# Kernel tuning notes

Hardware: AMD Instinct MI355X
Metric: run time of the kernel (lower is better)

Reference implementation:

```python
import jax, jax.numpy as jnp
import numpy as np

D_MODEL = 1024
HEADS = 16


def setup_inputs() -> dict:
    key = jax.random.key(0)
    ks = jax.random.split(key, 5)
    S = 4096
    x = jax.random.normal(ks[0], (S, D_MODEL), dtype=jnp.float32)
    scale = 1.0 / np.sqrt(D_MODEL)
    Wq = jax.random.normal(ks[1], (D_MODEL, D_MODEL), dtype=jnp.float32) * scale
    Wk = jax.random.normal(ks[2], (D_MODEL, D_MODEL), dtype=jnp.float32) * scale
    Wv = jax.random.normal(ks[3], (D_MODEL, D_MODEL), dtype=jnp.float32) * scale
    Wo = jax.random.normal(ks[4], (D_MODEL, D_MODEL), dtype=jnp.float32) * scale
    return {"x": x, "Wq": Wq, "Wk": Wk, "Wv": Wv, "Wo": Wo}


def reference(x, Wq, Wk, Wv, Wo):
    # x: [S, D]; weights follow torch Linear convention y = x @ W.T
    S, D = x.shape
    H = HEADS
    d_k = D // H
    q = (x @ Wq.T).reshape(S, H, d_k)  # [S,H,dk]
    k = (x @ Wk.T).reshape(S, H, d_k)
    v = (x @ Wv.T).reshape(S, H, d_k)
    # logits: [H, S, S] = q k^T / sqrt(d_k)
    logits = jnp.einsum('shd,thd->hst', q, k) / jnp.sqrt(jnp.asarray(d_k, x.dtype))
    probs = jax.nn.softmax(logits, axis=-1)
    out = jnp.einsum('hst,thd->shd', probs, v).reshape(S, D)
    return out @ Wo.T
```

## Files before the change

### kernel.cpp

```cpp
#include <hip/hip_runtime.h>
#include <hip/hip_bf16.h>


typedef __bf16 bf16_t;
typedef __bf16 bf16x8 __attribute__((ext_vector_type(8)));
typedef __bf16 bf16x4 __attribute__((ext_vector_type(4)));
typedef float f32x4 __attribute__((ext_vector_type(4)));

#define D_MODEL 1024
#define SEQ 4096
#define HEADS 16
#define DK 64
#define QSCALE 0.1803368801111204f
#define EXP2_MAGIC 8404859.0f

__global__ void cast_all(const float* __restrict__ x, const float* __restrict__ a,
                         const float* __restrict__ b, const float* __restrict__ c,
                         const float* __restrict__ d, bf16_t* __restrict__ xb,
                         bf16_t* __restrict__ wb) {
    const int gi = blockIdx.x * blockDim.x + threadIdx.x;
    const float* src; bf16_t* dst; int i;
    if (gi < SEQ * D_MODEL / 4) {
        src = x; dst = xb; i = gi * 4;
    } else {
        int g = gi - SEQ * D_MODEL / 4;
        int which = g >> 18;
        src = which == 0 ? a : which == 1 ? b : which == 2 ? c : d;
        dst = wb + (size_t)which * D_MODEL * D_MODEL;
        i = (g & 0x3FFFF) * 4;
    }
    float4 v = *(const float4*)(src + i);
    bf16x4 o;
    o[0] = (bf16_t)v.x; o[1] = (bf16_t)v.y; o[2] = (bf16_t)v.z; o[3] = (bf16_t)v.w;
    *(bf16x4*)(dst + i) = o;
}

__device__ __forceinline__ void g2l16(const bf16_t* g, bf16_t* l) {
    __builtin_amdgcn_global_load_lds(
        (const __attribute__((address_space(1))) void*)g,
        (__attribute__((address_space(3))) void*)l, 16, 0, 0);
}

__device__ __forceinline__ bf16x8 exp2_pk(const f32x4 a, const f32x4 b) {
    union { float f; unsigned u; } v[8];
#pragma unroll
    for (int r = 0; r < 4; r++) {
        v[r].f     = fmaf(a[r], 128.0f, EXP2_MAGIC);
        v[r + 4].f = fmaf(b[r], 128.0f, EXP2_MAGIC);
    }
    union { unsigned u[4]; bf16x8 h; } o;
#pragma unroll
    for (int p = 0; p < 4; p++)
        o.u[p] = __builtin_amdgcn_perm(v[2 * p + 1].u, v[2 * p].u, 0x05040100u);
    return o.h;
}

template <int ROUTE>
__global__ __launch_bounds__(256, 2) void gemm_lds(const bf16_t* __restrict__ A,
                                                   const bf16_t* __restrict__ B,
                                                   void* __restrict__ out0,
                                                   void* __restrict__ out1,
                                                   void* __restrict__ out2,
                                                   int M, int N, int K) {
    __shared__ __align__(16) bf16_t As[128 * 64];
    __shared__ __align__(16) bf16_t Bs[128 * 64];

    const int tid = threadIdx.x;
    const int lane = tid & 63;
    const int wave = tid >> 6;
    const int l15 = lane & 15;
    const int lg  = lane >> 4;

    const int flat = blockIdx.y * gridDim.x + blockIdx.x;
    const int mpx  = gridDim.y >> 3;
    const int xcd  = flat & 7;
    const int pos  = flat >> 3;
    const int m0 = (xcd * mpx + (pos % mpx)) * 128;
    const int n0 = (pos / mpx) * 128;
    const int wm = (wave >> 1) * 64;
    const int wn = (wave & 1) * 64;

    const bf16_t* aSrc[4]; bf16_t* aDst[4];
    const bf16_t* bSrc[4]; bf16_t* bDst[4];
#pragma unroll
    for (int it = 0; it < 4; it++) {
        int c = it * 256 + tid;
        int row = c >> 3, cc = (c & 7) ^ (row & 7);
        aSrc[it] = A + (size_t)(m0 + row) * K + cc * 8;
        aDst[it] = As + c * 8;
        bSrc[it] = B + (size_t)(n0 + row) * K + cc * 8;
        bDst[it] = Bs + c * 8;
    }

    int aoff[2][4], boff[2][4];
#pragma unroll
    for (int kk = 0; kk < 2; kk++) {
#pragma unroll
        for (int i = 0; i < 4; i++) {
            int row = wm + i * 16 + l15;
            aoff[kk][i] = row * 64 + (((kk << 2) | lg) ^ (row & 7)) * 8;
        }
#pragma unroll
        for (int j = 0; j < 4; j++) {
            int row = wn + j * 16 + l15;
            boff[kk][j] = row * 64 + (((kk << 2) | lg) ^ (row & 7)) * 8;
        }
    }

    f32x4 acc[4][4];
#pragma unroll
    for (int i = 0; i < 4; i++)
#pragma unroll
        for (int j = 0; j < 4; j++) acc[i][j] = f32x4{0.f, 0.f, 0.f, 0.f};

    for (int k0 = 0; k0 < K; k0 += 64) {
#pragma unroll
        for (int it = 0; it < 4; it++) g2l16(aSrc[it] + k0, aDst[it]);
#pragma unroll
        for (int it = 0; it < 4; it++) g2l16(bSrc[it] + k0, bDst[it]);
        __syncthreads();

#pragma unroll
        for (int kk = 0; kk < 2; kk++) {
            bf16x8 af[4], bfm[4];
#pragma unroll
            for (int i = 0; i < 4; i++) af[i] = *(const bf16x8*)(As + aoff[kk][i]);
#pragma unroll
            for (int j = 0; j < 4; j++) bfm[j] = *(const bf16x8*)(Bs + boff[kk][j]);
#pragma unroll
            for (int i = 0; i < 4; i++)
#pragma unroll
                for (int j = 0; j < 4; j++)
                    acc[i][j] = __builtin_amdgcn_mfma_f32_16x16x32_bf16(af[i], bfm[j], acc[i][j], 0, 0, 0);
        }
        __syncthreads();
    }

    const int ng = n0 + wn;
    if (ROUTE == 0) {
        float* C = (float*)out0;
#pragma unroll
        for (int i = 0; i < 4; i++)
#pragma unroll
            for (int r = 0; r < 4; r++) {
                int m = m0 + wm + i * 16 + lg * 4 + r;
                float* crow = C + (size_t)m * N + ng;
#pragma unroll
                for (int j = 0; j < 4; j++) crow[j * 16 + l15] = acc[i][j][r];
            }
    } else {
        if (ng < 2048) {
            const bool isQ = (ng < 1024);
            const float sc = isQ ? QSCALE : 1.0f;
            bf16_t* dst = isQ ? (bf16_t*)out0 : (bf16_t*)out1;
            int nn = ng & 1023;
#pragma unroll
            for (int i = 0; i < 4; i++)
#pragma unroll
                for (int r = 0; r < 4; r++) {
                    int m = m0 + wm + i * 16 + lg * 4 + r;
                    bf16_t* crow = dst + (size_t)m * D_MODEL + nn;
#pragma unroll
                    for (int j = 0; j < 4; j++) crow[j * 16 + l15] = (bf16_t)(acc[i][j][r] * sc);
                }
        } else {
            bf16_t* Vt = (bf16_t*)out2;
#pragma unroll
            for (int i = 0; i < 4; i++)
#pragma unroll
                for (int j = 0; j < 4; j++) {
                    int vcol = ng - 2048 + j * 16 + l15;
                    int m = m0 + wm + i * 16 + lg * 4;
                    int mp = (m & ~31) | (((m >> 2) & 3) << 3) | (((m >> 4) & 1) << 2);
                    bf16x4 v4;
#pragma unroll
                    for (int r = 0; r < 4; r++) v4[r] = (bf16_t)acc[i][j][r];
                    *(bf16x4*)(Vt + (size_t)vcol * SEQ + mp) = v4;
                }
        }
    }
}

__global__ __launch_bounds__(512, 2) void attn_kernel(const bf16_t* __restrict__ Q,
                                                      const bf16_t* __restrict__ Km,
                                                      const bf16_t* __restrict__ Vt,
                                                      bf16_t* __restrict__ O) {
    const int tid = threadIdx.x;
    const int lane = tid & 63;
    const int wave = tid >> 6;
    const int l15 = lane & 15;
    const int lg  = lane >> 4;
    const int bid = blockIdx.x;
    const int h    = (bid & 7) * 2 + ((bid >> 3) & 1);
    const int qblk = bid >> 4;
    const int q0 = qblk * 256;
    const int hoff = h * DK;

    __shared__ struct {
        __align__(16) bf16_t K[2][64 * 64];
        __align__(16) bf16_t V[2][64 * 64];
    } sm;

    bf16x8 qf[2][2];
#pragma unroll
    for (int t = 0; t < 2; t++)
#pragma unroll
        for (int c = 0; c < 2; c++)
            qf[t][c] = *(const bf16x8*)(Q + (size_t)(q0 + wave * 32 + t * 16 + l15) * D_MODEL
                                        + hoff + c * 32 + lg * 8);

    f32x4 oacc[2][4], lfrag[2];
#pragma unroll
    for (int t = 0; t < 2; t++) {
        lfrag[t] = f32x4{0.f, 0.f, 0.f, 0.f};
#pragma unroll
        for (int dt = 0; dt < 4; dt++) oacc[t][dt] = f32x4{0.f, 0.f, 0.f, 0.f};
    }

    bf16x8 ones8;
#pragma unroll
    for (int j = 0; j < 8; j++) ones8[j] = (bf16_t)1.0f;

    const int srow = tid >> 3;
    const int sdc = (tid & 7) ^ (srow & 7);
    const bf16_t* kSrc = Km + (size_t)srow * D_MODEL + hoff + sdc * 8;
    const bf16_t* vSrc = Vt + (size_t)(hoff + srow) * SEQ + sdc * 8;

    int kOff[4][2], vOff[2][4];
#pragma unroll
    for (int kt = 0; kt < 4; kt++)
#pragma unroll
        for (int c = 0; c < 2; c++) {
            int row = kt * 16 + l15;
            kOff[kt][c] = row * 64 + (((c * 4 + lg) ^ (row & 7)) * 8);
        }
#pragma unroll
    for (int kp = 0; kp < 2; kp++)
#pragma unroll
        for (int dt = 0; dt < 4; dt++) {
            int row = dt * 16 + l15;
            vOff[kp][dt] = row * 64 + (((kp * 4 + lg) ^ (row & 7)) * 8);
        }

    g2l16(kSrc, &sm.K[0][tid * 8]);
    g2l16(vSrc, &sm.V[0][tid * 8]);

    for (int s = 0; s < SEQ / 64; s++) {
        const int cur = s & 1;
        __syncthreads();

        if (s + 1 < SEQ / 64) {
            const int nxt = cur ^ 1;
            g2l16(kSrc + (size_t)(s + 1) * 64 * D_MODEL, &sm.K[nxt][tid * 8]);
            g2l16(vSrc + (s + 1) * 64,                   &sm.V[nxt][tid * 8]);
        }

        const bf16_t* Kb = sm.K[cur];
        const bf16_t* Vb = sm.V[cur];

#pragma unroll
        for (int kp = 0; kp < 2; kp++) {
            bf16x8 vf[4];
#pragma unroll
            for (int dt = 0; dt < 4; dt++) vf[dt] = *(const bf16x8*)(Vb + vOff[kp][dt]);

            f32x4 st[2][2];
#pragma unroll
            for (int sub = 0; sub < 2; sub++) {
                const int kt = kp * 2 + sub;
                const bf16x8 kf0 = *(const bf16x8*)(Kb + kOff[kt][0]);
                const bf16x8 kf1 = *(const bf16x8*)(Kb + kOff[kt][1]);
#pragma unroll
                for (int t = 0; t < 2; t++) {
                    f32x4 a = f32x4{0.f, 0.f, 0.f, 0.f};
                    a = __builtin_amdgcn_mfma_f32_16x16x32_bf16(kf0, qf[t][0], a, 0, 0, 0);
                    a = __builtin_amdgcn_mfma_f32_16x16x32_bf16(kf1, qf[t][1], a, 0, 0, 0);
                    st[t][sub] = a;
                }
            }

#pragma unroll
            for (int t = 0; t < 2; t++) {
                const bf16x8 pbig = exp2_pk(st[t][0], st[t][1]);
                lfrag[t] = __builtin_amdgcn_mfma_f32_16x16x32_bf16(ones8, pbig, lfrag[t], 0, 0, 0);
#pragma unroll
                for (int dt = 0; dt < 4; dt++)
                    oacc[t][dt] = __builtin_amdgcn_mfma_f32_16x16x32_bf16(vf[dt], pbig, oacc[t][dt], 0, 0, 0);
            }
        }
    }

#pragma unroll
    for (int t = 0; t < 2; t++) {
        const float inv = 1.f / lfrag[t][0];
        const size_t qrow = (size_t)(q0 + wave * 32 + t * 16 + l15);
#pragma unroll
        for (int dt = 0; dt < 4; dt++) {
            bf16x4 o4;
#pragma unroll
            for (int r = 0; r < 4; r++) o4[r] = (bf16_t)(oacc[t][dt][r] * inv);
            *(bf16x4*)(O + qrow * D_MODEL + hoff + dt * 16 + lg * 4) = o4;
        }
    }
}

extern "C" void kernel_launch(void* const* d_in, const int* in_sizes, int n_in,
                              void* d_out, int out_size, void* d_ws, size_t ws_size,
                              hipStream_t stream) {
    const float* x  = (const float*)d_in[0];
    const float* Wq = (const float*)d_in[1];
    const float* Wk = (const float*)d_in[2];
    const float* Wv = (const float*)d_in[3];
    const float* Wo = (const float*)d_in[4];
    float* out = (float*)d_out;

    char* ws = (char*)d_ws;
    bf16_t* xb  = (bf16_t*)(ws);
    bf16_t* wqb = (bf16_t*)(ws + (8u  << 20));
    bf16_t* wob = (bf16_t*)(ws + (14u << 20));
    bf16_t* Qb  = (bf16_t*)(ws + (16u << 20));
    bf16_t* Kb  = (bf16_t*)(ws + (24u << 20));
    bf16_t* Vtb = (bf16_t*)(ws + (32u << 20));
    bf16_t* Ab  = (bf16_t*)(ws + (40u << 20));

    cast_all<<<8192, 256, 0, stream>>>(x, Wq, Wk, Wv, Wo, xb, wqb);

    gemm_lds<1><<<dim3(3 * D_MODEL / 128, SEQ / 128), 256, 0, stream>>>(
        xb, wqb, Qb, Kb, Vtb, SEQ, 3 * D_MODEL, D_MODEL);

    attn_kernel<<<256, 512, 0, stream>>>(Qb, Kb, Vtb, Ab);

    gemm_lds<0><<<dim3(D_MODEL / 128, SEQ / 128), 256, 0, stream>>>(
        Ab, wob, out, nullptr, nullptr, SEQ, D_MODEL, D_MODEL);
}
```

Baseline: 185.4 us.

## Fuse fp32-to-bf16 casts into GEMM tile loads and drop cast kernel

Removes the separate cast_all kernel and has the QKV and output-projection GEMMs read fp32 inputs and weights directly, converting to bf16 in registers before writing swizzled LDS tiles. This saves one launch and the write-then-reread of bf16 copies of x and the weights. The cost is twice the global read bytes per tile, repeated conversion work across the blocks that share a tile, and synchronous register-staged loads in place of the async global_load_lds path, which may stall the MFMA loop.

```diff
diff --git a/kernel.cpp b/kernel.cpp
--- a/kernel.cpp
+++ b/kernel.cpp
@@ -14,27 +14,6 @@
 #define QSCALE 0.1803368801111204f
 #define EXP2_MAGIC 8404859.0f
 
-__global__ void cast_all(const float* __restrict__ x, const float* __restrict__ a,
-                         const float* __restrict__ b, const float* __restrict__ c,
-                         const float* __restrict__ d, bf16_t* __restrict__ xb,
-                         bf16_t* __restrict__ wb) {
-    const int gi = blockIdx.x * blockDim.x + threadIdx.x;
-    const float* src; bf16_t* dst; int i;
-    if (gi < SEQ * D_MODEL / 4) {
-        src = x; dst = xb; i = gi * 4;
-    } else {
-        int g = gi - SEQ * D_MODEL / 4;
-        int which = g >> 18;
-        src = which == 0 ? a : which == 1 ? b : which == 2 ? c : d;
-        dst = wb + (size_t)which * D_MODEL * D_MODEL;
-        i = (g & 0x3FFFF) * 4;
-    }
-    float4 v = *(const float4*)(src + i);
-    bf16x4 o;
-    o[0] = (bf16_t)v.x; o[1] = (bf16_t)v.y; o[2] = (bf16_t)v.z; o[3] = (bf16_t)v.w;
-    *(bf16x4*)(dst + i) = o;
-}
-
 __device__ __forceinline__ void g2l16(const bf16_t* g, bf16_t* l) {
     __builtin_amdgcn_global_load_lds(
         (const __attribute__((address_space(1))) void*)g,
@@ -55,13 +34,21 @@
     return o.h;
 }
 
-template <int ROUTE>
-__global__ __launch_bounds__(256, 2) void gemm_lds(const bf16_t* __restrict__ A,
-                                                   const bf16_t* __restrict__ B,
-                                                   void* __restrict__ out0,
-                                                   void* __restrict__ out1,
-                                                   void* __restrict__ out2,
-                                                   int M, int N, int K) {
+__device__ __forceinline__ bf16x8 cvt8(const float4 p0, const float4 p1) {
+    bf16x8 w;
+    w[0] = (bf16_t)p0.x; w[1] = (bf16_t)p0.y; w[2] = (bf16_t)p0.z; w[3] = (bf16_t)p0.w;
+    w[4] = (bf16_t)p1.x; w[5] = (bf16_t)p1.y; w[6] = (bf16_t)p1.z; w[7] = (bf16_t)p1.w;
+    return w;
+}
+
+__global__ __launch_bounds__(256) void gemm_qkv(const float* __restrict__ X,
+                                                const float* __restrict__ Wq,
+                                                const float* __restrict__ Wk,
+                                                const float* __restrict__ Wv,
+                                                bf16_t* __restrict__ Qb,
+                                                bf16_t* __restrict__ Kb,
+                                                bf16_t* __restrict__ Vt) {
+    const int K = D_MODEL;
     __shared__ __align__(16) bf16_t As[128 * 64];
     __shared__ __align__(16) bf16_t Bs[128 * 64];
 
@@ -80,16 +67,19 @@
     const int wm = (wave >> 1) * 64;
     const int wn = (wave & 1) * 64;
 
-    const bf16_t* aSrc[4]; bf16_t* aDst[4];
-    const bf16_t* bSrc[4]; bf16_t* bDst[4];
+    const float* Wsel = (n0 < 1024) ? Wq : (n0 < 2048) ? Wk : Wv;
+    const int nb = n0 & 1023;
+
+    const float* aS[4]; const float* bS[4];
+    bf16_t* aD[4]; bf16_t* bD[4];
 #pragma unroll
     for (int it = 0; it < 4; it++) {
         int c = it * 256 + tid;
-        int row = c >> 3, cc = (c & 7) ^ (row & 7);
-        aSrc[it] = A + (size_t)(m0 + row) * K + cc * 8;
-        aDst[it] = As + c * 8;
-        bSrc[it] = B + (size_t)(n0 + row) * K + cc * 8;
-        bDst[it] = Bs + c * 8;
+        int row = c >> 3, j0 = c & 7, cc = j0 ^ (row & 7);
+        aS[it] = X    + (size_t)(m0 + row) * K + j0 * 8;
+        bS[it] = Wsel + (size_t)(nb + row) * K + j0 * 8;
+        aD[it] = As + row * 64 + cc * 8;
+        bD[it] = Bs + row * 64 + cc * 8;
     }
 
     int aoff[2][4], boff[2][4];
@@ -115,9 +105,17 @@
 
     for (int k0 = 0; k0 < K; k0 += 64) {
 #pragma unroll
-        for (int it = 0; it < 4; it++) g2l16(aSrc[it] + k0, aDst[it]);
-#pragma unroll
-        for (int it = 0; it < 4; it++) g2l16(bSrc[it] + k0, bDst[it]);
+        for (int it = 0; it < 4; it++) {
+            float4 p0 = *(const float4*)(aS[it] + k0);
+            float4 p1 = *(const float4*)(aS[it] + k0 + 4);
+            *(bf16x8*)aD[it] = cvt8(p0, p1);
+        }
+#pragma unroll
+        for (int it = 0; it < 4; it++) {
+            float4 p0 = *(const float4*)(bS[it] + k0);
+            float4 p1 = *(const float4*)(bS[it] + k0 + 4);
+            *(bf16x8*)bD[it] = cvt8(p0, p1);
+        }
         __syncthreads();
 
 #pragma unroll
@@ -137,48 +135,128 @@
     }
 
     const int ng = n0 + wn;
-    if (ROUTE == 0) {
-        float* C = (float*)out0;
+    if (ng < 2048) {
+        const bool isQ = (ng < 1024);
+        const float sc = isQ ? QSCALE : 1.0f;
+        bf16_t* dst = isQ ? Qb : Kb;
+        int nn = ng & 1023;
 #pragma unroll
         for (int i = 0; i < 4; i++)
 #pragma unroll
             for (int r = 0; r < 4; r++) {
                 int m = m0 + wm + i * 16 + lg * 4 + r;
-                float* crow = C + (size_t)m * N + ng;
-#pragma unroll
-                for (int j = 0; j < 4; j++) crow[j * 16 + l15] = acc[i][j][r];
+                bf16_t* crow = dst + (size_t)m * D_MODEL + nn;
+#pragma unroll
+                for (int j = 0; j < 4; j++) crow[j * 16 + l15] = (bf16_t)(acc[i][j][r] * sc);
             }
     } else {
-        if (ng < 2048) {
-            const bool isQ = (ng < 1024);
-            const float sc = isQ ? QSCALE : 1.0f;
-            bf16_t* dst = isQ ? (bf16_t*)out0 : (bf16_t*)out1;
-            int nn = ng & 1023;
+#pragma unroll
+        for (int i = 0; i < 4; i++)
+#pragma unroll
+            for (int j = 0; j < 4; j++) {
+                int vcol = ng - 2048 + j * 16 + l15;
+                int m = m0 + wm + i * 16 + lg * 4;
+                int mp = (m & ~31) | (((m >> 2) & 3) << 3) | (((m >> 4) & 1) << 2);
+                bf16x4 v4;
+#pragma unroll
+                for (int r = 0; r < 4; r++) v4[r] = (bf16_t)acc[i][j][r];
+                *(bf16x4*)(Vt + (size_t)vcol * SEQ + mp) = v4;
+            }
+    }
+}
+
+__global__ __launch_bounds__(256) void gemm_out(const bf16_t* __restrict__ A,
+                                                const float* __restrict__ Wo,
+                                                float* __restrict__ C) {
+    const int K = D_MODEL, N = D_MODEL;
+    __shared__ __align__(16) bf16_t As[128 * 64];
+    __shared__ __align__(16) bf16_t Bs[128 * 64];
+
+    const int tid = threadIdx.x;
+    const int lane = tid & 63;
+    const int wave = tid >> 6;
+    const int l15 = lane & 15;
+    const int lg  = lane >> 4;
+
+    const int flat = blockIdx.y * gridDim.x + blockIdx.x;
+    const int mpx  = gridDim.y >> 3;
+    const int xcd  = flat & 7;
+    const int pos  = flat >> 3;
+    const int m0 = (xcd * mpx + (pos % mpx)) * 128;
+    const int n0 = (pos / mpx) * 128;
+    const int wm = (wave >> 1) * 64;
+    const int wn = (wave & 1) * 64;
+
+    const bf16_t* aSrc[4]; bf16_t* aDst[4];
+    const float* bS[4]; bf16_t* bD[4];
+#pragma unroll
+    for (int it = 0; it < 4; it++) {
+        int c = it * 256 + tid;
+        int row = c >> 3, j0 = c & 7, cc = j0 ^ (row & 7);
+        aSrc[it] = A + (size_t)(m0 + row) * K + cc * 8;
+        aDst[it] = As + c * 8;
+        bS[it] = Wo + (size_t)(n0 + row) * K + j0 * 8;
+        bD[it] = Bs + row * 64 + cc * 8;
+    }
+
+    int aoff[2][4], boff[2][4];
+#pragma unroll
+    for (int kk = 0; kk < 2; kk++) {
+#pragma unroll
+        for (int i = 0; i < 4; i++) {
+            int row = wm + i * 16 + l15;
+            aoff[kk][i] = row * 64 + (((kk << 2) | lg) ^ (row & 7)) * 8;
+        }
+#pragma unroll
+        for (int j = 0; j < 4; j++) {
+            int row = wn + j * 16 + l15;
+            boff[kk][j] = row * 64 + (((kk << 2) | lg) ^ (row & 7)) * 8;
+        }
+    }
+
+    f32x4 acc[4][4];
+#pragma unroll
+    for (int i = 0; i < 4; i++)
+#pragma unroll
+        for (int j = 0; j < 4; j++) acc[i][j] = f32x4{0.f, 0.f, 0.f, 0.f};
+
+    for (int k0 = 0; k0 < K; k0 += 64) {
+#pragma unroll
+        for (int it = 0; it < 4; it++) g2l16(aSrc[it] + k0, aDst[it]);
+#pragma unroll
+        for (int it = 0; it < 4; it++) {
+            float4 p0 = *(const float4*)(bS[it] + k0);
+            float4 p1 = *(const float4*)(bS[it] + k0 + 4);
+            *(bf16x8*)bD[it] = cvt8(p0, p1);
+        }
+        __syncthreads();
+
+#pragma unroll
+        for (int kk = 0; kk < 2; kk++) {
+            bf16x8 af[4], bfm[4];
+#pragma unroll
+            for (int i = 0; i < 4; i++) af[i] = *(const bf16x8*)(As + aoff[kk][i]);
+#pragma unroll
+            for (int j = 0; j < 4; j++) bfm[j] = *(const bf16x8*)(Bs + boff[kk][j]);
 #pragma unroll
             for (int i = 0; i < 4; i++)
 #pragma unroll
-                for (int r = 0; r < 4; r++) {
-                    int m = m0 + wm + i * 16 + lg * 4 + r;
-                    bf16_t* crow = dst + (size_t)m * D_MODEL + nn;
-#pragma unroll
-                    for (int j = 0; j < 4; j++) crow[j * 16 + l15] = (bf16_t)(acc[i][j][r] * sc);
-                }
-        } else {
-            bf16_t* Vt = (bf16_t*)out2;
-#pragma unroll
-            for (int i = 0; i < 4; i++)
-#pragma unroll
-                for (int j = 0; j < 4; j++) {
-                    int vcol = ng - 2048 + j * 16 + l15;
-                    int m = m0 + wm + i * 16 + lg * 4;
-                    int mp = (m & ~31) | (((m >> 2) & 3) << 3) | (((m >> 4) & 1) << 2);
-                    bf16x4 v4;
-#pragma unroll
-                    for (int r = 0; r < 4; r++) v4[r] = (bf16_t)acc[i][j][r];
-                    *(bf16x4*)(Vt + (size_t)vcol * SEQ + mp) = v4;
-                }
-        }
-    }
+                for (int j = 0; j < 4; j++)
+                    acc[i][j] = __builtin_amdgcn_mfma_f32_16x16x32_bf16(af[i], bfm[j], acc[i][j], 0, 0, 0);
+        }
+        __syncthreads();
+    }
+
+    const int ng = n0 + wn;
+#pragma unroll
+    for (int i = 0; i < 4; i++)
+#pragma unroll
+        for (int r = 0; r < 4; r++) {
+            int m = m0 + wm + i * 16 + lg * 4 + r;
+            float* crow = C + (size_t)m * N + ng;
+#pragma unroll
+            for (int j = 0; j < 4; j++) crow[j * 16 + l15] = acc[i][j][r];
+        }
 }
 
 __global__ __launch_bounds__(512, 2) void attn_kernel(const bf16_t* __restrict__ Q,
@@ -315,21 +393,15 @@
     float* out = (float*)d_out;
 
     char* ws = (char*)d_ws;
-    bf16_t* xb  = (bf16_t*)(ws);
-    bf16_t* wqb = (bf16_t*)(ws + (8u  << 20));
-    bf16_t* wob = (bf16_t*)(ws + (14u << 20));
     bf16_t* Qb  = (bf16_t*)(ws + (16u << 20));
     bf16_t* Kb  = (bf16_t*)(ws + (24u << 20));
     bf16_t* Vtb = (bf16_t*)(ws + (32u << 20));
     bf16_t* Ab  = (bf16_t*)(ws + (40u << 20));
 
-    cast_all<<<8192, 256, 0, stream>>>(x, Wq, Wk, Wv, Wo, xb, wqb);
-
-    gemm_lds<1><<<dim3(3 * D_MODEL / 128, SEQ / 128), 256, 0, stream>>>(
-        xb, wqb, Qb, Kb, Vtb, SEQ, 3 * D_MODEL, D_MODEL);
+    gemm_qkv<<<dim3(3 * D_MODEL / 128, SEQ / 128), 256, 0, stream>>>(
+        x, Wq, Wk, Wv, Qb, Kb, Vtb);
 
     attn_kernel<<<256, 512, 0, stream>>>(Qb, Kb, Vtb, Ab);
 
-    gemm_lds<0><<<dim3(D_MODEL / 128, SEQ / 128), 256, 0, stream>>>(
-        Ab, wob, out, nullptr, nullptr, SEQ, D_MODEL, D_MODEL);
-}
+    gemm_out<<<dim3(D_MODEL / 128, SEQ / 128), 256, 0, stream>>>(Ab, Wo, out);
+}
```

Result: slower. 227.9 us (+22.9%).

## Double-buffer LDS tiles in projection GEMM to overlap loads with MFMA

Applied to the files above, without the earlier changes.

The projection GEMM now uses two LDS buffers for the A and B tiles. The next K-slice is prefetched into the spare buffer right after the barrier, while MFMAs run on the current buffer. This also drops the trailing barrier, so each K step has one barrier instead of two, and global-to-LDS latency is meant to hide behind compute. The cost is twice the LDS per block (64KB), which may limit occupancy under the two-blocks-per-CU launch bound. The GEMMs are only part of the total time alongside attention.

```diff
diff --git a/kernel.cpp b/kernel.cpp
--- a/kernel.cpp
+++ b/kernel.cpp
@@ -62,8 +62,8 @@
                                                    void* __restrict__ out1,
                                                    void* __restrict__ out2,
                                                    int M, int N, int K) {
-    __shared__ __align__(16) bf16_t As[128 * 64];
-    __shared__ __align__(16) bf16_t Bs[128 * 64];
+    __shared__ __align__(16) bf16_t As[2][128 * 64];
+    __shared__ __align__(16) bf16_t Bs[2][128 * 64];
 
     const int tid = threadIdx.x;
     const int lane = tid & 63;
@@ -80,16 +80,15 @@
     const int wm = (wave >> 1) * 64;
     const int wn = (wave & 1) * 64;
 
-    const bf16_t* aSrc[4]; bf16_t* aDst[4];
-    const bf16_t* bSrc[4]; bf16_t* bDst[4];
+    const bf16_t* aSrc[4]; const bf16_t* bSrc[4];
+    int sOff[4];
 #pragma unroll
     for (int it = 0; it < 4; it++) {
         int c = it * 256 + tid;
         int row = c >> 3, cc = (c & 7) ^ (row & 7);
         aSrc[it] = A + (size_t)(m0 + row) * K + cc * 8;
-        aDst[it] = As + c * 8;
         bSrc[it] = B + (size_t)(n0 + row) * K + cc * 8;
-        bDst[it] = Bs + c * 8;
+        sOff[it] = c * 8;
     }
 
     int aoff[2][4], boff[2][4];
@@ -113,27 +112,40 @@
 #pragma unroll
         for (int j = 0; j < 4; j++) acc[i][j] = f32x4{0.f, 0.f, 0.f, 0.f};
 
-    for (int k0 = 0; k0 < K; k0 += 64) {
-#pragma unroll
-        for (int it = 0; it < 4; it++) g2l16(aSrc[it] + k0, aDst[it]);
-#pragma unroll
-        for (int it = 0; it < 4; it++) g2l16(bSrc[it] + k0, bDst[it]);
+#pragma unroll
+    for (int it = 0; it < 4; it++) g2l16(aSrc[it], &As[0][sOff[it]]);
+#pragma unroll
+    for (int it = 0; it < 4; it++) g2l16(bSrc[it], &Bs[0][sOff[it]]);
+
+    const int nsteps = K / 64;
+    for (int s = 0; s < nsteps; s++) {
+        const int cur = s & 1;
         __syncthreads();
 
+        if (s + 1 < nsteps) {
+            const int nxt = cur ^ 1;
+            const int k1 = (s + 1) * 64;
+#pragma unroll
+            for (int it = 0; it < 4; it++) g2l16(aSrc[it] + k1, &As[nxt][sOff[it]]);
+#pragma unroll
+            for (int it = 0; it < 4; it++) g2l16(bSrc[it] + k1, &Bs[nxt][sOff[it]]);
+        }
+
+        const bf16_t* Ab_ = As[cur];
+        const bf16_t* Bb_ = Bs[cur];
 #pragma unroll
         for (int kk = 0; kk < 2; kk++) {
             bf16x8 af[4], bfm[4];
 #pragma unroll
-            for (int i = 0; i < 4; i++) af[i] = *(const bf16x8*)(As + aoff[kk][i]);
-#pragma unroll
-            for (int j = 0; j < 4; j++) bfm[j] = *(const bf16x8*)(Bs + boff[kk][j]);
+            for (int i = 0; i < 4; i++) af[i] = *(const bf16x8*)(Ab_ + aoff[kk][i]);
+#pragma unroll
+            for (int j = 0; j < 4; j++) bfm[j] = *(const bf16x8*)(Bb_ + boff[kk][j]);
 #pragma unroll
             for (int i = 0; i < 4; i++)
 #pragma unroll
                 for (int j = 0; j < 4; j++)
                     acc[i][j] = __builtin_amdgcn_mfma_f32_16x16x32_bf16(af[i], bfm[j], acc[i][j], 0, 0, 0);
         }
-        __syncthreads();
     }
 
     const int ng = n0 + wn;
```

Result: slower. 195.6 us (+5.5%).

## Split attention KV range across two wave groups with 64 query rows per wave

Applied to the files above, without the earlier changes.

Each wave now handles 64 query rows instead of 32. The 8 waves form two groups that each process half of the key/value sequence, using separate double-buffered K/V tiles in shared memory. At the end the partial outputs and row sums are combined through a shared scratch buffer. This gives more MFMA work per K/V fragment loaded from LDS and halves the loop trip count. The cost is more registers (accumulators double), a larger shared memory footprint, and an extra reduction step, which may lower occupancy under the 512x2 launch bounds.

```diff
diff --git a/kernel.cpp b/kernel.cpp
--- a/kernel.cpp
+++ b/kernel.cpp
@@ -188,6 +188,8 @@
     const int tid = threadIdx.x;
     const int lane = tid & 63;
     const int wave = tid >> 6;
+    const int gw   = wave & 3;
+    const int grp  = wave >> 2;
     const int l15 = lane & 15;
     const int lg  = lane >> 4;
     const int bid = blockIdx.x;
@@ -196,22 +198,28 @@
     const int q0 = qblk * 256;
     const int hoff = h * DK;
 
-    __shared__ struct {
-        __align__(16) bf16_t K[2][64 * 64];
-        __align__(16) bf16_t V[2][64 * 64];
+    __shared__ union {
+        struct {
+            __align__(16) bf16_t Klo[2][64 * 64];
+            __align__(16) bf16_t Vlo[2][64 * 64];
+            __align__(16) bf16_t Khi[2][64 * 64];
+            __align__(16) bf16_t Vhi[2][64 * 64];
+        } kv;
+        float scratch[4][64][68];
     } sm;
-
-    bf16x8 qf[2][2];
-#pragma unroll
-    for (int t = 0; t < 2; t++)
+    __shared__ float lsum[4][64];
+
+    bf16x8 qf[4][2];
+#pragma unroll
+    for (int t = 0; t < 4; t++)
 #pragma unroll
         for (int c = 0; c < 2; c++)
-            qf[t][c] = *(const bf16x8*)(Q + (size_t)(q0 + wave * 32 + t * 16 + l15) * D_MODEL
+            qf[t][c] = *(const bf16x8*)(Q + (size_t)(q0 + gw * 64 + t * 16 + l15) * D_MODEL
                                         + hoff + c * 32 + lg * 8);
 
-    f32x4 oacc[2][4], lfrag[2];
-#pragma unroll
-    for (int t = 0; t < 2; t++) {
+    f32x4 oacc[4][4], lfrag[4];
+#pragma unroll
+    for (int t = 0; t < 4; t++) {
         lfrag[t] = f32x4{0.f, 0.f, 0.f, 0.f};
 #pragma unroll
         for (int dt = 0; dt < 4; dt++) oacc[t][dt] = f32x4{0.f, 0.f, 0.f, 0.f};
@@ -225,6 +233,8 @@
     const int sdc = (tid & 7) ^ (srow & 7);
     const bf16_t* kSrc = Km + (size_t)srow * D_MODEL + hoff + sdc * 8;
     const bf16_t* vSrc = Vt + (size_t)(hoff + srow) * SEQ + sdc * 8;
+    const size_t kHi = (size_t)32 * 64 * D_MODEL;
+    const int    vHi = 2048;
 
     int kOff[4][2], vOff[2][4];
 #pragma unroll
@@ -242,21 +252,27 @@
             vOff[kp][dt] = row * 64 + (((kp * 4 + lg) ^ (row & 7)) * 8);
         }
 
-    g2l16(kSrc, &sm.K[0][tid * 8]);
-    g2l16(vSrc, &sm.V[0][tid * 8]);
-
-    for (int s = 0; s < SEQ / 64; s++) {
+    g2l16(kSrc,       &sm.kv.Klo[0][tid * 8]);
+    g2l16(vSrc,       &sm.kv.Vlo[0][tid * 8]);
+    g2l16(kSrc + kHi, &sm.kv.Khi[0][tid * 8]);
+    g2l16(vSrc + vHi, &sm.kv.Vhi[0][tid * 8]);
+
+    for (int s = 0; s < 32; s++) {
         const int cur = s & 1;
         __syncthreads();
 
-        if (s + 1 < SEQ / 64) {
+        if (s + 1 < 32) {
             const int nxt = cur ^ 1;
-            g2l16(kSrc + (size_t)(s + 1) * 64 * D_MODEL, &sm.K[nxt][tid * 8]);
-            g2l16(vSrc + (s + 1) * 64,                   &sm.V[nxt][tid * 8]);
-        }
-
-        const bf16_t* Kb = sm.K[cur];
-        const bf16_t* Vb = sm.V[cur];
+            const size_t ko = (size_t)(s + 1) * 64 * D_MODEL;
+            const int    vo = (s + 1) * 64;
+            g2l16(kSrc + ko,       &sm.kv.Klo[nxt][tid * 8]);
+            g2l16(vSrc + vo,       &sm.kv.Vlo[nxt][tid * 8]);
+            g2l16(kSrc + kHi + ko, &sm.kv.Khi[nxt][tid * 8]);
+            g2l16(vSrc + vHi + vo, &sm.kv.Vhi[nxt][tid * 8]);
+        }
+
+        const bf16_t* Kb = grp ? sm.kv.Khi[cur] : sm.kv.Klo[cur];
+        const bf16_t* Vb = grp ? sm.kv.Vhi[cur] : sm.kv.Vlo[cur];
 
 #pragma unroll
         for (int kp = 0; kp < 2; kp++) {
@@ -264,14 +280,14 @@
 #pragma unroll
             for (int dt = 0; dt < 4; dt++) vf[dt] = *(const bf16x8*)(Vb + vOff[kp][dt]);
 
-            f32x4 st[2][2];
+            f32x4 st[4][2];
 #pragma unroll
             for (int sub = 0; sub < 2; sub++) {
                 const int kt = kp * 2 + sub;
                 const bf16x8 kf0 = *(const bf16x8*)(Kb + kOff[kt][0]);
                 const bf16x8 kf1 = *(const bf16x8*)(Kb + kOff[kt][1]);
 #pragma unroll
-                for (int t = 0; t < 2; t++) {
+                for (int t = 0; t < 4; t++) {
                     f32x4 a = f32x4{0.f, 0.f, 0.f, 0.f};
                     a = __builtin_amdgcn_mfma_f32_16x16x32_bf16(kf0, qf[t][0], a, 0, 0, 0);
                     a = __builtin_amdgcn_mfma_f32_16x16x32_bf16(kf1, qf[t][1], a, 0, 0, 0);
@@ -280,7 +296,7 @@
             }
 
 #pragma unroll
-            for (int t = 0; t < 2; t++) {
+            for (int t = 0; t < 4; t++) {
                 const bf16x8 pbig = exp2_pk(st[t][0], st[t][1]);
                 lfrag[t] = __builtin_amdgcn_mfma_f32_16x16x32_bf16(ones8, pbig, lfrag[t], 0, 0, 0);
 #pragma unroll
@@ -290,16 +306,31 @@
         }
     }
 
-#pragma unroll
-    for (int t = 0; t < 2; t++) {
-        const float inv = 1.f / lfrag[t][0];
-        const size_t qrow = (size_t)(q0 + wave * 32 + t * 16 + l15);
-#pragma unroll
-        for (int dt = 0; dt < 4; dt++) {
-            bf16x4 o4;
-#pragma unroll
-            for (int r = 0; r < 4; r++) o4[r] = (bf16_t)(oacc[t][dt][r] * inv);
-            *(bf16x4*)(O + qrow * D_MODEL + hoff + dt * 16 + lg * 4) = o4;
+    __syncthreads();
+    if (grp == 1) {
+#pragma unroll
+        for (int t = 0; t < 4; t++) {
+#pragma unroll
+            for (int dt = 0; dt < 4; dt++)
+                *(f32x4*)&sm.scratch[gw][t * 16 + l15][dt * 16 + lg * 4] = oacc[t][dt];
+            if (lg == 0) lsum[gw][t * 16 + l15] = lfrag[t][0];
+        }
+    }
+    __syncthreads();
+    if (grp == 0) {
+#pragma unroll
+        for (int t = 0; t < 4; t++) {
+            const float l = lfrag[t][0] + lsum[gw][t * 16 + l15];
+            const float inv = 1.f / l;
+            const size_t qrow = (size_t)(q0 + gw * 64 + t * 16 + l15);
+#pragma unroll
+            for (int dt = 0; dt < 4; dt++) {
+                f32x4 oh = *(const f32x4*)&sm.scratch[gw][t * 16 + l15][dt * 16 + lg * 4];
+                bf16x4 o4;
+#pragma unroll
+                for (int r = 0; r < 4; r++) o4[r] = (bf16_t)((oacc[t][dt][r] + oh[r]) * inv);
+                *(bf16x4*)(O + qrow * D_MODEL + hoff + dt * 16 + lg * 4) = o4;
+            }
         }
     }
 }
```

After: 199.2 us. 7.4% more time.
